# Kernel optimization log

Hardware: AMD Instinct MI355X
Metric: run time of the kernel (lower is better)

Reference implementation:

```python
import jax, jax.numpy as jnp
import numpy as np

N = 100000   # nodes
E = 1200000  # edges
F_IN = 16    # input node features
H = 64       # hidden dim (hard-coded in GinNet)
G = 1024     # graphs in the batch
BN_EPS = 1e-5


def setup_inputs() -> dict:
    key = jax.random.key(0)
    ks = jax.random.split(key, 16)

    def dense(k, shape):
        return (jax.random.normal(k, shape, jnp.float32) * (1.0 / np.sqrt(shape[0]))).astype(jnp.float32)

    x = jax.random.normal(ks[0], (N, F_IN), jnp.float32)
    edge_index = jax.random.randint(ks[1], (2, E), 0, N)
    batch = jnp.sort(jax.random.randint(ks[2], (N,), 0, G))

    inp = {
        'x': x, 'edge_index': edge_index, 'batch': batch,
        # GIN layer 1 (MLP F_IN->H->H, eps, BN affine)
        'W1a': dense(ks[3], (F_IN, H)), 'b1a': jnp.zeros((H,), jnp.float32),
        'W1b': dense(ks[4], (H, H)),    'b1b': jnp.zeros((H,), jnp.float32),
        'eps1': jnp.zeros((), jnp.float32), 'g1': jnp.ones((H,), jnp.float32), 'be1': jnp.zeros((H,), jnp.float32),
        # GIN layer 2
        'W2a': dense(ks[5], (H, H)), 'b2a': jnp.zeros((H,), jnp.float32),
        'W2b': dense(ks[6], (H, H)), 'b2b': jnp.zeros((H,), jnp.float32),
        'eps2': jnp.zeros((), jnp.float32), 'g2': jnp.ones((H,), jnp.float32), 'be2': jnp.zeros((H,), jnp.float32),
        # GIN layer 3
        'W3a': dense(ks[7], (H, H)), 'b3a': jnp.zeros((H,), jnp.float32),
        'W3b': dense(ks[8], (H, H)), 'b3b': jnp.zeros((H,), jnp.float32),
        'eps3': jnp.zeros((), jnp.float32), 'g3': jnp.ones((H,), jnp.float32), 'be3': jnp.zeros((H,), jnp.float32),
        # readout MLP
        'Wf1': dense(ks[9], (H, 10)), 'bf1': jnp.zeros((10,), jnp.float32),
        'Wf2': dense(ks[10], (10, 1)), 'bf2': jnp.zeros((1,), jnp.float32),
    }
    return inp


def _gin_bn(x, edge_index, eps, Wa, ba, Wb, bb, gamma, beta):
    # GINConv: out = MLP((1+eps)*x + sum_{j->i} x_j)
    msgs = x[edge_index[0]]                                      # [E, d] gather
    aggr = jax.ops.segment_sum(msgs, edge_index[1], num_segments=N)  # [N, d] scatter-add
    h = (1.0 + eps) * x + aggr
    h = jnp.maximum(h @ Wa + ba, 0.0) @ Wb + bb                  # Linear-ReLU-Linear
    h = jnp.maximum(h, 0.0)                                      # F.relu after conv
    # BatchNorm1d in training mode: batch statistics (biased var)
    mu = h.mean(axis=0)
    var = h.var(axis=0)
    return gamma * (h - mu) * jax.lax.rsqrt(var + BN_EPS) + beta


def reference(x, edge_index, batch,
              W1a, b1a, W1b, b1b, eps1, g1, be1,
              W2a, b2a, W2b, b2b, eps2, g2, be2,
              W3a, b3a, W3b, b3b, eps3, g3, be3,
              Wf1, bf1, Wf2, bf2):
    h = _gin_bn(x, edge_index, eps1, W1a, b1a, W1b, b1b, g1, be1)
    h = _gin_bn(h, edge_index, eps2, W2a, b2a, W2b, b2b, g2, be2)
    h = _gin_bn(h, edge_index, eps3, W3a, b3a, W3b, b3b, g3, be3)
    # global_mean_pool over graph ids
    sums = jax.ops.segment_sum(h, batch, num_segments=G)                     # [G, H]
    cnt = jax.ops.segment_sum(jnp.ones((N,), jnp.float32), batch, num_segments=G)
    pooled = sums / jnp.maximum(cnt, 1.0)[:, None]
    h = jnp.maximum(pooled @ Wf1 + bf1, 0.0)
    return h @ Wf2 + bf2  # [G, 1]
```

## Files before the change

### kernel.cpp

```cpp
#include <hip/hip_runtime.h>
#include <hip/hip_bf16.h>


#define HD 64
#define NBLK 256
#define BSH 9

typedef unsigned short u16;

__device__ __forceinline__ float bf2f(u16 u) {
    return __uint_as_float(((unsigned int)u) << 16);
}
__device__ __forceinline__ u16 f2bf(float f) {
    unsigned int u = __float_as_uint(f);
    unsigned int r = 0x7FFFu + ((u >> 16) & 1u);
    return (u16)((u + r) >> 16);
}

__global__ void hist_kernel(const int* __restrict__ ei, int* __restrict__ ghist, int E, int C) {
    __shared__ int lh[256];
    int b = blockIdx.x, tid = threadIdx.x;
    lh[tid] = 0;
    __syncthreads();
    int beg = b * C, end = min(beg + C, E);
    for (int i = beg + tid; i < end; i += 256) atomicAdd(&lh[ei[E + i] >> BSH], 1);
    __syncthreads();
    ghist[b * 256 + tid] = lh[tid];
}

__global__ void colscan_kernel(int* __restrict__ ghist, int* __restrict__ total) {
    __shared__ int s[256];
    int k = blockIdx.x, b = threadIdx.x;
    int v = ghist[b * 256 + k];
    s[b] = v;
    __syncthreads();
    for (int off = 1; off < 256; off <<= 1) {
        int u = (b >= off) ? s[b - off] : 0;
        __syncthreads();
        s[b] += u;
        __syncthreads();
    }
    ghist[b * 256 + k] = s[b] - v;
    if (b == 255) total[k] = s[255];
}

__global__ void base_kernel(const int* __restrict__ total, int* __restrict__ bbase, int NBUCK) {
    __shared__ int s[256];
    int t = threadIdx.x;
    int v = (t < NBUCK) ? total[t] : 0;
    s[t] = v;
    __syncthreads();
    for (int off = 1; off < 256; off <<= 1) {
        int u = (t >= off) ? s[t - off] : 0;
        __syncthreads();
        s[t] += u;
        __syncthreads();
    }
    if (t == 0) bbase[0] = 0;
    bbase[t + 1] = s[t];
}

__global__ void scatter_kernel(const int* __restrict__ ei, const int* __restrict__ ghist,
                               const int* __restrict__ bbase, int* __restrict__ bpack,
                               int E, int C) {
    __shared__ int lcur[256];
    int b = blockIdx.x, tid = threadIdx.x;
    lcur[tid] = bbase[tid] + ghist[b * 256 + tid];
    __syncthreads();
    int beg = b * C, end = min(beg + C, E);
    for (int i = beg + tid; i < end; i += 256) {
        int src = ei[i], dst = ei[E + i];
        int pos = atomicAdd(&lcur[dst >> BSH], 1);
        bpack[pos] = src | ((dst & 511) << 17);
    }
}

__global__ void csrbuild_kernel(const int* __restrict__ bpack, const int* __restrict__ bbase,
                                int* __restrict__ row_start, int* __restrict__ csr, int N) {
    __shared__ int h[512], s[512], lc[512];
    int k = blockIdx.x, tid = threadIdx.x;
    int beg = bbase[k], end = bbase[k + 1];
    h[tid] = 0; h[tid + 256] = 0;
    __syncthreads();
    for (int i = beg + tid; i < end; i += 256) atomicAdd(&h[(bpack[i] >> 17) & 511], 1);
    __syncthreads();
    s[tid] = h[tid]; s[tid + 256] = h[tid + 256];
    __syncthreads();
    for (int off = 1; off < 512; off <<= 1) {
        int v0 = (tid >= off) ? s[tid - off] : 0;
        int t1 = tid + 256;
        int v1 = (t1 >= off) ? s[t1 - off] : 0;
        __syncthreads();
        s[tid] += v0; s[t1] += v1;
        __syncthreads();
    }
    int e0 = s[tid] - h[tid], e1 = s[tid + 256] - h[tid + 256];
    lc[tid] = e0; lc[tid + 256] = e1;
    int n0 = (k << BSH) + tid, n1 = (k << BSH) + tid + 256;
    if (n0 < N) row_start[n0] = beg + e0;
    if (n1 < N) row_start[n1] = beg + e1;
    if (k == gridDim.x - 1 && tid == 0) row_start[N] = end;
    __syncthreads();
    for (int i = beg + tid; i < end; i += 256) {
        int v = bpack[i];
        int pos = beg + atomicAdd(&lc[(v >> 17) & 511], 1);
        csr[pos] = v & 0x1FFFF;
    }
}

__global__ void gather64_kernel(const u16* __restrict__ x, const int* __restrict__ rs,
                                const int* __restrict__ csr, float* __restrict__ aggr, int N) {
    int lane = threadIdx.x & 63;
    int l4 = lane & 15;
    int wave = (blockIdx.x * blockDim.x + threadIdx.x) >> 6;
    int n = wave * 4 + (lane >> 4);
    if (n >= N) return;
    int beg = rs[n], end = rs[n + 1];
    const u16* xb = x + (size_t)l4 * 4;
    float a0x = 0, a0y = 0, a0z = 0, a0w = 0;
    float a1x = 0, a1y = 0, a1z = 0, a1w = 0;
    float a2x = 0, a2y = 0, a2z = 0, a2w = 0;
    float a3x = 0, a3y = 0, a3z = 0, a3w = 0;
    for (int base = beg; base < end; base += 16) {
        int cnt = end - base; if (cnt > 16) cnt = 16;
        int e = (l4 < cnt) ? csr[base + l4] : 0;
        int j = 0;
        for (; j + 4 <= cnt; j += 4) {
            int s0 = __shfl(e, j + 0, 16);
            int s1 = __shfl(e, j + 1, 16);
            int s2 = __shfl(e, j + 2, 16);
            int s3 = __shfl(e, j + 3, 16);
            ushort4 u0 = *(const ushort4*)(xb + (size_t)s0 * 64);
            ushort4 u1 = *(const ushort4*)(xb + (size_t)s1 * 64);
            ushort4 u2 = *(const ushort4*)(xb + (size_t)s2 * 64);
            ushort4 u3 = *(const ushort4*)(xb + (size_t)s3 * 64);
            a0x += bf2f(u0.x); a0y += bf2f(u0.y); a0z += bf2f(u0.z); a0w += bf2f(u0.w);
            a1x += bf2f(u1.x); a1y += bf2f(u1.y); a1z += bf2f(u1.z); a1w += bf2f(u1.w);
            a2x += bf2f(u2.x); a2y += bf2f(u2.y); a2z += bf2f(u2.z); a2w += bf2f(u2.w);
            a3x += bf2f(u3.x); a3y += bf2f(u3.y); a3z += bf2f(u3.z); a3w += bf2f(u3.w);
        }
        for (; j < cnt; j++) {
            int s = __shfl(e, j, 16);
            ushort4 u = *(const ushort4*)(xb + (size_t)s * 64);
            a0x += bf2f(u.x); a0y += bf2f(u.y); a0z += bf2f(u.z); a0w += bf2f(u.w);
        }
    }
    float4 o;
    o.x = (a0x + a1x) + (a2x + a3x);
    o.y = (a0y + a1y) + (a2y + a3y);
    o.z = (a0z + a1z) + (a2z + a3z);
    o.w = (a0w + a1w) + (a2w + a3w);
    *reinterpret_cast<float4*>(aggr + (size_t)n * 64 + l4 * 4) = o;
}

__global__ void gather16_kernel(const float* __restrict__ x, const int* __restrict__ rs,
                                const int* __restrict__ csr, float* __restrict__ aggr, int N) {
    int lane = threadIdx.x & 63;
    int l4 = lane & 3;
    int wave = (blockIdx.x * blockDim.x + threadIdx.x) >> 6;
    int n = wave * 16 + (lane >> 2);
    if (n >= N) return;
    int beg = rs[n], end = rs[n + 1];
    const float* xb = x + (size_t)l4 * 4;
    float a0x = 0, a0y = 0, a0z = 0, a0w = 0;
    float a1x = 0, a1y = 0, a1z = 0, a1w = 0;
    float a2x = 0, a2y = 0, a2z = 0, a2w = 0;
    float a3x = 0, a3y = 0, a3z = 0, a3w = 0;
    for (int base = beg; base < end; base += 4) {
        int cnt = end - base; if (cnt > 4) cnt = 4;
        int e = (l4 < cnt) ? csr[base + l4] : 0;
        if (cnt == 4) {
            int s0 = __shfl(e, 0, 4);
            int s1 = __shfl(e, 1, 4);
            int s2 = __shfl(e, 2, 4);
            int s3 = __shfl(e, 3, 4);
            float4 v0 = *(const float4*)(xb + (size_t)s0 * 16);
            float4 v1 = *(const float4*)(xb + (size_t)s1 * 16);
            float4 v2 = *(const float4*)(xb + (size_t)s2 * 16);
            float4 v3 = *(const float4*)(xb + (size_t)s3 * 16);
            a0x += v0.x; a0y += v0.y; a0z += v0.z; a0w += v0.w;
            a1x += v1.x; a1y += v1.y; a1z += v1.z; a1w += v1.w;
            a2x += v2.x; a2y += v2.y; a2z += v2.z; a2w += v2.w;
            a3x += v3.x; a3y += v3.y; a3z += v3.z; a3w += v3.w;
        } else {
            for (int j = 0; j < cnt; j++) {
                int s = __shfl(e, j, 4);
                float4 v = *(const float4*)(xb + (size_t)s * 16);
                a0x += v.x; a0y += v.y; a0z += v.z; a0w += v.w;
            }
        }
    }
    float4 o;
    o.x = (a0x + a1x) + (a2x + a3x);
    o.y = (a0y + a1y) + (a2y + a3y);
    o.z = (a0z + a1z) + (a2z + a3z);
    o.w = (a0w + a1w) + (a2w + a3w);
    *reinterpret_cast<float4*>(aggr + (size_t)n * 16 + l4 * 4) = o;
}

template <int DIN, bool AFF>
__launch_bounds__(256)
__global__ void fused_mlp_kernel(const void* __restrict__ xin_, const float* __restrict__ aggr,
                                 const int* __restrict__ rs,
                                 const float* __restrict__ Wa, const float* __restrict__ ba,
                                 const float* __restrict__ Wb, const float* __restrict__ bb,
                                 const float* __restrict__ epsp,
                                 const float* __restrict__ statsPrev,
                                 const float* __restrict__ gPrev, const float* __restrict__ bePrev,
                                 u16* __restrict__ hout, float* __restrict__ stats, int N) {
    __shared__ float Wa_s[DIN * 64];
    __shared__ float Wb_s[64 * 64];
    __shared__ float zts[64 * 68];
    __shared__ float statS[128];
    __shared__ float degS[64];
    __shared__ float aS[64], cS[64], uS[64];

    const int tid = threadIdx.x;
    const int tc = tid & 15;
    const int tn = tid >> 4;
    const float* xinF = (const float*)xin_;
    const u16*   xinB = (const u16*)xin_;

    if (AFF) {
        if (tid < 64) {
            float invN = 1.0f / (float)N;
            float mu = statsPrev[tid] * invN;
            float var = statsPrev[64 + tid] * invN - mu * mu;
            float inv = rsqrtf(var + 1e-5f);
            float a = gPrev[tid] * inv;
            aS[tid] = a;
            cS[tid] = bePrev[tid] - mu * a;
        }
        __syncthreads();
        for (int i = tid; i < DIN * 64; i += 256) Wa_s[i] = aS[i >> 6] * Wa[i];
        if (tid < 64) {
            float s = 0.0f;
            for (int k = 0; k < 64; k++) s = fmaf(cS[k], Wa[k * 64 + tid], s);
            uS[tid] = s;
        }
    } else {
        for (int i = tid; i < DIN * 64; i += 256) Wa_s[i] = Wa[i];
    }
    for (int i = tid; i < 64 * 64; i += 256) Wb_s[i] = Wb[i];
    if (tid < 128) statS[tid] = 0.0f;
    const float e1 = 1.0f + epsp[0];
    __syncthreads();

    float4 t4;
    t4 = *(const float4*)&ba[tc * 4];
    const float bav[4] = {t4.x, t4.y, t4.z, t4.w};
    t4 = *(const float4*)&bb[tc * 4];
    const float bbv[4] = {t4.x, t4.y, t4.z, t4.w};
    float uv[4] = {0, 0, 0, 0};
    if (AFF) { uv[0] = uS[tc * 4]; uv[1] = uS[tc * 4 + 1]; uv[2] = uS[tc * 4 + 2]; uv[3] = uS[tc * 4 + 3]; }

    float sv[4] = {0, 0, 0, 0}, qv[4] = {0, 0, 0, 0};

    const int ITER = 2;
    int blockBase = blockIdx.x * (64 * ITER);
    for (int it = 0; it < ITER; ++it) {
        int gbase = blockBase + it * 64;
        float zr[4][4];
        if (DIN == 64) {
#pragma unroll
            for (int i = 0; i < 4; ++i) {
                int node = gbase + tn * 4 + i;
                float4 av = {0, 0, 0, 0};
                float xf[4] = {0, 0, 0, 0};
                if (node < N) {
                    ushort4 xu = *(const ushort4*)&xinB[(size_t)node * 64 + tc * 4];
                    xf[0] = bf2f(xu.x); xf[1] = bf2f(xu.y); xf[2] = bf2f(xu.z); xf[3] = bf2f(xu.w);
                    av = *(const float4*)&aggr[(size_t)node * 64 + tc * 4];
                }
                zr[i][0] = fmaf(e1, xf[0], av.x);
                zr[i][1] = fmaf(e1, xf[1], av.y);
                zr[i][2] = fmaf(e1, xf[2], av.z);
                zr[i][3] = fmaf(e1, xf[3], av.w);
            }
        } else {
            int node = gbase + tn * 4 + (tc >> 2);
            float4 xv = {0, 0, 0, 0}, av = {0, 0, 0, 0};
            if (node < N) {
                xv = *(const float4*)&xinF[(size_t)node * 16 + (tc & 3) * 4];
                av = *(const float4*)&aggr[(size_t)node * 16 + (tc & 3) * 4];
            }
            zr[0][0] = fmaf(e1, xv.x, av.x);
            zr[0][1] = fmaf(e1, xv.y, av.y);
            zr[0][2] = fmaf(e1, xv.z, av.z);
            zr[0][3] = fmaf(e1, xv.w, av.w);
        }
        float dg[4];
        if (AFF && tid < 64) {
            int node = gbase + tid;
            degS[tid] = (node < N) ? (float)(rs[node + 1] - rs[node]) : 0.0f;
        }
        __syncthreads();
        if (DIN == 64) {
#pragma unroll
            for (int j = 0; j < 4; ++j) {
                float4 w = {zr[0][j], zr[1][j], zr[2][j], zr[3][j]};
                *(float4*)&zts[(tc * 4 + j) * 68 + tn * 4] = w;
            }
        } else {
#pragma unroll
            for (int j = 0; j < 4; ++j)
                zts[((tc & 3) * 4 + j) * 68 + tn * 4 + (tc >> 2)] = zr[0][j];
        }
        __syncthreads();
        if (AFF) {
#pragma unroll
            for (int i = 0; i < 4; ++i) dg[i] = e1 + degS[tn * 4 + i];
        }
        float ac[4][4];
#pragma unroll
        for (int i = 0; i < 4; ++i)
#pragma unroll
            for (int j = 0; j < 4; ++j)
                ac[i][j] = AFF ? fmaf(dg[i], uv[j], bav[j]) : bav[j];
#pragma unroll 8
        for (int k = 0; k < DIN; ++k) {
            float4 zv = *(const float4*)&zts[k * 68 + tn * 4];
            float4 wv = *(const float4*)&Wa_s[k * 64 + tc * 4];
            const float zf[4] = {zv.x, zv.y, zv.z, zv.w};
            const float wf[4] = {wv.x, wv.y, wv.z, wv.w};
#pragma unroll
            for (int i = 0; i < 4; ++i)
#pragma unroll
                for (int j = 0; j < 4; ++j)
                    ac[i][j] = fmaf(zf[i], wf[j], ac[i][j]);
        }
#pragma unroll
        for (int i = 0; i < 4; ++i)
#pragma unroll
            for (int j = 0; j < 4; ++j)
                ac[i][j] = fmaxf(ac[i][j], 0.0f);
        __syncthreads();
#pragma unroll
        for (int j = 0; j < 4; ++j) {
            float4 w = {ac[0][j], ac[1][j], ac[2][j], ac[3][j]};
            *(float4*)&zts[(tc * 4 + j) * 68 + tn * 4] = w;
        }
        __syncthreads();
        float hc[4][4];
#pragma unroll
        for (int i = 0; i < 4; ++i)
#pragma unroll
            for (int j = 0; j < 4; ++j)
                hc[i][j] = bbv[j];
#pragma unroll 8
        for (int k = 0; k < 64; ++k) {
            float4 tv = *(const float4*)&zts[k * 68 + tn * 4];
            float4 wv = *(const float4*)&Wb_s[k * 64 + tc * 4];
            const float tf[4] = {tv.x, tv.y, tv.z, tv.w};
            const float wf[4] = {wv.x, wv.y, wv.z, wv.w};
#pragma unroll
            for (int i = 0; i < 4; ++i)
#pragma unroll
                for (int j = 0; j < 4; ++j)
                    hc[i][j] = fmaf(tf[i], wf[j], hc[i][j]);
        }
#pragma unroll
        for (int i = 0; i < 4; ++i) {
            int node = gbase + tn * 4 + i;
            if (node < N) {
                float o0 = fmaxf(hc[i][0], 0.0f), o1 = fmaxf(hc[i][1], 0.0f);
                float o2 = fmaxf(hc[i][2], 0.0f), o3 = fmaxf(hc[i][3], 0.0f);
                ushort4 ob = {f2bf(o0), f2bf(o1), f2bf(o2), f2bf(o3)};
                *(ushort4*)&hout[(size_t)node * 64 + tc * 4] = ob;
                sv[0] += o0; sv[1] += o1; sv[2] += o2; sv[3] += o3;
                qv[0] += o0 * o0; qv[1] += o1 * o1; qv[2] += o2 * o2; qv[3] += o3 * o3;
            }
        }
    }
#pragma unroll
    for (int off = 16; off < 64; off <<= 1) {
#pragma unroll
        for (int j = 0; j < 4; ++j) {
            sv[j] += __shfl_xor(sv[j], off);
            qv[j] += __shfl_xor(qv[j], off);
        }
    }
    if ((tid & 63) < 16) {
#pragma unroll
        for (int j = 0; j < 4; ++j) {
            atomicAdd(&statS[tc * 4 + j], sv[j]);
            atomicAdd(&statS[64 + tc * 4 + j], qv[j]);
        }
    }
    __syncthreads();
    if (tid < 128) unsafeAtomicAdd(&stats[tid], statS[tid]);
}

__global__ void pool_seg_kernel(const u16* __restrict__ h, const int* __restrict__ batch,
                                float* __restrict__ pool, float* __restrict__ cnt, int N) {
    int lane = threadIdx.x & 63;
    int wave = (blockIdx.x * blockDim.x + threadIdx.x) >> 6;
    int base = wave * 16;
    if (base >= N) return;
    int end = base + 16; if (end > N) end = N;
    int cur = batch[base];
    float acc = 0.0f;
    int run = 0;
    for (int n = base; n < end; n++) {
        int gid = batch[n];
        if (gid != cur) {
            unsafeAtomicAdd(&pool[(size_t)cur * 64 + lane], acc);
            if (lane == 0) unsafeAtomicAdd(&cnt[cur], (float)run);
            acc = 0.0f; run = 0; cur = gid;
        }
        acc += bf2f(h[(size_t)n * 64 + lane]);
        run++;
    }
    unsafeAtomicAdd(&pool[(size_t)cur * 64 + lane], acc);
    if (lane == 0) unsafeAtomicAdd(&cnt[cur], (float)run);
}

__global__ void readout_kernel(const float* __restrict__ pool, const float* __restrict__ cnt,
                               const float* __restrict__ stats, const float* __restrict__ g3,
                               const float* __restrict__ be3,
                               const float* __restrict__ Wf1, const float* __restrict__ bf1,
                               const float* __restrict__ Wf2, const float* __restrict__ bf2,
                               float* __restrict__ out, int N) {
    int gb = blockIdx.x;
    int t = threadIdx.x;
    float invN = 1.0f / (float)N;
    float mu = stats[t] * invN;
    float var = stats[64 + t] * invN - mu * mu;
    float inv = rsqrtf(var + 1e-5f);
    float a = g3[t] * inv;
    float c = be3[t] - mu * a;
    float cn = cnt[gb];
    float p = (cn > 0.0f) ? (a * (pool[(size_t)gb * 64 + t] / cn) + c) : 0.0f;
    float o = 0.0f;
#pragma unroll
    for (int j = 0; j < 10; j++) {
        float part = p * Wf1[t * 10 + j];
#pragma unroll
        for (int off = 32; off > 0; off >>= 1) part += __shfl_down(part, off);
        float z = fmaxf(part + bf1[j], 0.0f);
        o = fmaf(z, Wf2[j], o);
    }
    if (t == 0) out[gb] = o + bf2[0];
}

extern "C" void kernel_launch(void* const* d_in, const int* in_sizes, int n_in,
                              void* d_out, int out_size, void* d_ws, size_t ws_size,
                              hipStream_t stream) {
    const float* x      = (const float*)d_in[0];
    const int*   ei     = (const int*)d_in[1];
    const int*   batch  = (const int*)d_in[2];
    const float* W1a = (const float*)d_in[3];  const float* b1a = (const float*)d_in[4];
    const float* W1b = (const float*)d_in[5];  const float* b1b = (const float*)d_in[6];
    const float* e1  = (const float*)d_in[7];  const float* g1  = (const float*)d_in[8];
    const float* be1 = (const float*)d_in[9];
    const float* W2a = (const float*)d_in[10]; const float* b2a = (const float*)d_in[11];
    const float* W2b = (const float*)d_in[12]; const float* b2b = (const float*)d_in[13];
    const float* e2  = (const float*)d_in[14]; const float* g2  = (const float*)d_in[15];
    const float* be2 = (const float*)d_in[16];
    const float* W3a = (const float*)d_in[17]; const float* b3a = (const float*)d_in[18];
    const float* W3b = (const float*)d_in[19]; const float* b3b = (const float*)d_in[20];
    const float* e3  = (const float*)d_in[21]; const float* g3  = (const float*)d_in[22];
    const float* be3 = (const float*)d_in[23];
    const float* Wf1 = (const float*)d_in[24]; const float* bf1 = (const float*)d_in[25];
    const float* Wf2 = (const float*)d_in[26]; const float* bf2 = (const float*)d_in[27];

    const int N = in_sizes[2];
    const int E = in_sizes[1] / 2;
    const int G = out_size;
    const int NBUCK = (N + 511) >> BSH;
    const int C = (E + NBLK - 1) / NBLK;

    int* csr       = (int*)d_ws;
    int* row_start = csr + E;
    int* bpack     = row_start + N + 64;
    int* ghist     = bpack + E;
    int* total     = ghist + NBLK * 256;
    int* bbase     = total + 256;
    float* stats   = (float*)(bbase + 272);
    float* pool    = stats + 384;
    float* cnt     = pool + (size_t)G * HD;
    float* aggr    = cnt + G;
    size_t NH = (size_t)N * HD;
    u16* hA        = (u16*)(aggr + NH);
    u16* hB        = hA + NH;

    const int TB = 256;
    int fusedGrid = (N + 127) / 128;
    size_t zeroBytes = (size_t)(384 + (size_t)G * HD + G) * sizeof(float);

    hipMemsetAsync(stats, 0, zeroBytes, stream);
    hist_kernel<<<NBLK, 256, 0, stream>>>(ei, ghist, E, C);
    colscan_kernel<<<NBUCK, 256, 0, stream>>>(ghist, total);
    base_kernel<<<1, 256, 0, stream>>>(total, bbase, NBUCK);
    scatter_kernel<<<NBLK, 256, 0, stream>>>(ei, ghist, bbase, bpack, E, C);
    csrbuild_kernel<<<NBUCK, 256, 0, stream>>>(bpack, bbase, row_start, csr, N);

    gather16_kernel<<<((N + 15) / 16 * 64 + TB - 1) / TB, TB, 0, stream>>>(x, row_start, csr, aggr, N);
    fused_mlp_kernel<16, false><<<fusedGrid, TB, 0, stream>>>(
        x, aggr, row_start, W1a, b1a, W1b, b1b, e1, nullptr, nullptr, nullptr, hA, stats, N);

    gather64_kernel<<<((N + 3) / 4 * 64 + TB - 1) / TB, TB, 0, stream>>>(hA, row_start, csr, aggr, N);
    fused_mlp_kernel<64, true><<<fusedGrid, TB, 0, stream>>>(
        hA, aggr, row_start, W2a, b2a, W2b, b2b, e2, stats, g1, be1, hB, stats + 128, N);

    gather64_kernel<<<((N + 3) / 4 * 64 + TB - 1) / TB, TB, 0, stream>>>(hB, row_start, csr, aggr, N);
    fused_mlp_kernel<64, true><<<fusedGrid, TB, 0, stream>>>(
        hB, aggr, row_start, W3a, b3a, W3b, b3b, e3, stats + 128, g2, be2, hA, stats + 256, N);

    int poolWaves = (N + 15) / 16;
    pool_seg_kernel<<<(poolWaves * 64 + TB - 1) / TB, TB, 0, stream>>>(hA, batch, pool, cnt, N);
    readout_kernel<<<G, 64, 0, stream>>>(pool, cnt, stats + 256, g3, be3,
                                         Wf1, bf1, Wf2, bf2, (float*)d_out, N);
}
```

Measured before the change: 406.6 us.

## Fuse neighbor gather-aggregation into the fused MLP kernel

Removes the separate gather16/gather64 kernels and performs the CSR neighbor sum directly inside fused_mlp_kernel, feeding the result straight into the MLP. This eliminates writing and re-reading the fp32 aggr buffer (N×64 floats per layer) and three kernel launches. In exchange, the gather now runs at the MLP kernel's occupancy and block shape (256 threads, large shared memory), and each thread handles four nodes serially, which may expose gather latency and load imbalance across degree variation.

New measurement: 442.2 us. 8.8% more time.

```diff
diff --git a/kernel.cpp b/kernel.cpp
--- a/kernel.cpp
+++ b/kernel.cpp
@@ -108,100 +108,10 @@
     }
 }
 
-__global__ void gather64_kernel(const u16* __restrict__ x, const int* __restrict__ rs,
-                                const int* __restrict__ csr, float* __restrict__ aggr, int N) {
-    int lane = threadIdx.x & 63;
-    int l4 = lane & 15;
-    int wave = (blockIdx.x * blockDim.x + threadIdx.x) >> 6;
-    int n = wave * 4 + (lane >> 4);
-    if (n >= N) return;
-    int beg = rs[n], end = rs[n + 1];
-    const u16* xb = x + (size_t)l4 * 4;
-    float a0x = 0, a0y = 0, a0z = 0, a0w = 0;
-    float a1x = 0, a1y = 0, a1z = 0, a1w = 0;
-    float a2x = 0, a2y = 0, a2z = 0, a2w = 0;
-    float a3x = 0, a3y = 0, a3z = 0, a3w = 0;
-    for (int base = beg; base < end; base += 16) {
-        int cnt = end - base; if (cnt > 16) cnt = 16;
-        int e = (l4 < cnt) ? csr[base + l4] : 0;
-        int j = 0;
-        for (; j + 4 <= cnt; j += 4) {
-            int s0 = __shfl(e, j + 0, 16);
-            int s1 = __shfl(e, j + 1, 16);
-            int s2 = __shfl(e, j + 2, 16);
-            int s3 = __shfl(e, j + 3, 16);
-            ushort4 u0 = *(const ushort4*)(xb + (size_t)s0 * 64);
-            ushort4 u1 = *(const ushort4*)(xb + (size_t)s1 * 64);
-            ushort4 u2 = *(const ushort4*)(xb + (size_t)s2 * 64);
-            ushort4 u3 = *(const ushort4*)(xb + (size_t)s3 * 64);
-            a0x += bf2f(u0.x); a0y += bf2f(u0.y); a0z += bf2f(u0.z); a0w += bf2f(u0.w);
-            a1x += bf2f(u1.x); a1y += bf2f(u1.y); a1z += bf2f(u1.z); a1w += bf2f(u1.w);
-            a2x += bf2f(u2.x); a2y += bf2f(u2.y); a2z += bf2f(u2.z); a2w += bf2f(u2.w);
-            a3x += bf2f(u3.x); a3y += bf2f(u3.y); a3z += bf2f(u3.z); a3w += bf2f(u3.w);
-        }
-        for (; j < cnt; j++) {
-            int s = __shfl(e, j, 16);
-            ushort4 u = *(const ushort4*)(xb + (size_t)s * 64);
-            a0x += bf2f(u.x); a0y += bf2f(u.y); a0z += bf2f(u.z); a0w += bf2f(u.w);
-        }
-    }
-    float4 o;
-    o.x = (a0x + a1x) + (a2x + a3x);
-    o.y = (a0y + a1y) + (a2y + a3y);
-    o.z = (a0z + a1z) + (a2z + a3z);
-    o.w = (a0w + a1w) + (a2w + a3w);
-    *reinterpret_cast<float4*>(aggr + (size_t)n * 64 + l4 * 4) = o;
-}
-
-__global__ void gather16_kernel(const float* __restrict__ x, const int* __restrict__ rs,
-                                const int* __restrict__ csr, float* __restrict__ aggr, int N) {
-    int lane = threadIdx.x & 63;
-    int l4 = lane & 3;
-    int wave = (blockIdx.x * blockDim.x + threadIdx.x) >> 6;
-    int n = wave * 16 + (lane >> 2);
-    if (n >= N) return;
-    int beg = rs[n], end = rs[n + 1];
-    const float* xb = x + (size_t)l4 * 4;
-    float a0x = 0, a0y = 0, a0z = 0, a0w = 0;
-    float a1x = 0, a1y = 0, a1z = 0, a1w = 0;
-    float a2x = 0, a2y = 0, a2z = 0, a2w = 0;
-    float a3x = 0, a3y = 0, a3z = 0, a3w = 0;
-    for (int base = beg; base < end; base += 4) {
-        int cnt = end - base; if (cnt > 4) cnt = 4;
-        int e = (l4 < cnt) ? csr[base + l4] : 0;
-        if (cnt == 4) {
-            int s0 = __shfl(e, 0, 4);
-            int s1 = __shfl(e, 1, 4);
-            int s2 = __shfl(e, 2, 4);
-            int s3 = __shfl(e, 3, 4);
-            float4 v0 = *(const float4*)(xb + (size_t)s0 * 16);
-            float4 v1 = *(const float4*)(xb + (size_t)s1 * 16);
-            float4 v2 = *(const float4*)(xb + (size_t)s2 * 16);
-            float4 v3 = *(const float4*)(xb + (size_t)s3 * 16);
-            a0x += v0.x; a0y += v0.y; a0z += v0.z; a0w += v0.w;
-            a1x += v1.x; a1y += v1.y; a1z += v1.z; a1w += v1.w;
-            a2x += v2.x; a2y += v2.y; a2z += v2.z; a2w += v2.w;
-            a3x += v3.x; a3y += v3.y; a3z += v3.z; a3w += v3.w;
-        } else {
-            for (int j = 0; j < cnt; j++) {
-                int s = __shfl(e, j, 4);
-                float4 v = *(const float4*)(xb + (size_t)s * 16);
-                a0x += v.x; a0y += v.y; a0z += v.z; a0w += v.w;
-            }
-        }
-    }
-    float4 o;
-    o.x = (a0x + a1x) + (a2x + a3x);
-    o.y = (a0y + a1y) + (a2y + a3y);
-    o.z = (a0z + a1z) + (a2z + a3z);
-    o.w = (a0w + a1w) + (a2w + a3w);
-    *reinterpret_cast<float4*>(aggr + (size_t)n * 16 + l4 * 4) = o;
-}
-
 template <int DIN, bool AFF>
 __launch_bounds__(256)
-__global__ void fused_mlp_kernel(const void* __restrict__ xin_, const float* __restrict__ aggr,
-                                 const int* __restrict__ rs,
+__global__ void fused_mlp_kernel(const void* __restrict__ xin_,
+                                 const int* __restrict__ rs, const int* __restrict__ csr,
                                  const float* __restrict__ Wa, const float* __restrict__ ba,
                                  const float* __restrict__ Wb, const float* __restrict__ bb,
                                  const float* __restrict__ epsp,
@@ -265,29 +175,89 @@
 #pragma unroll
             for (int i = 0; i < 4; ++i) {
                 int node = gbase + tn * 4 + i;
-                float4 av = {0, 0, 0, 0};
-                float xf[4] = {0, 0, 0, 0};
+                float a0x = 0, a0y = 0, a0z = 0, a0w = 0;
+                float a1x = 0, a1y = 0, a1z = 0, a1w = 0;
+                float a2x = 0, a2y = 0, a2z = 0, a2w = 0;
+                float a3x = 0, a3y = 0, a3z = 0, a3w = 0;
                 if (node < N) {
-                    ushort4 xu = *(const ushort4*)&xinB[(size_t)node * 64 + tc * 4];
-                    xf[0] = bf2f(xu.x); xf[1] = bf2f(xu.y); xf[2] = bf2f(xu.z); xf[3] = bf2f(xu.w);
-                    av = *(const float4*)&aggr[(size_t)node * 64 + tc * 4];
+                    int beg = rs[node], end = rs[node + 1];
+                    const u16* xb = xinB + (size_t)tc * 4;
+                    for (int base = beg; base < end; base += 16) {
+                        int cnt = end - base; if (cnt > 16) cnt = 16;
+                        int e = (tc < cnt) ? csr[base + tc] : 0;
+                        int j = 0;
+                        for (; j + 4 <= cnt; j += 4) {
+                            int s0 = __shfl(e, j + 0, 16);
+                            int s1 = __shfl(e, j + 1, 16);
+                            int s2 = __shfl(e, j + 2, 16);
+                            int s3 = __shfl(e, j + 3, 16);
+                            ushort4 u0 = *(const ushort4*)(xb + (size_t)s0 * 64);
+                            ushort4 u1 = *(const ushort4*)(xb + (size_t)s1 * 64);
+                            ushort4 u2 = *(const ushort4*)(xb + (size_t)s2 * 64);
+                            ushort4 u3 = *(const ushort4*)(xb + (size_t)s3 * 64);
+                            a0x += bf2f(u0.x); a0y += bf2f(u0.y); a0z += bf2f(u0.z); a0w += bf2f(u0.w);
+                            a1x += bf2f(u1.x); a1y += bf2f(u1.y); a1z += bf2f(u1.z); a1w += bf2f(u1.w);
+                            a2x += bf2f(u2.x); a2y += bf2f(u2.y); a2z += bf2f(u2.z); a2w += bf2f(u2.w);
+                            a3x += bf2f(u3.x); a3y += bf2f(u3.y); a3z += bf2f(u3.z); a3w += bf2f(u3.w);
+                        }
+                        for (; j < cnt; j++) {
+                            int s = __shfl(e, j, 16);
+                            ushort4 u = *(const ushort4*)(xb + (size_t)s * 64);
+                            a0x += bf2f(u.x); a0y += bf2f(u.y); a0z += bf2f(u.z); a0w += bf2f(u.w);
+                        }
+                    }
+                    ushort4 xs = *(const ushort4*)&xinB[(size_t)node * 64 + tc * 4];
+                    zr[i][0] = fmaf(e1, bf2f(xs.x), (a0x + a1x) + (a2x + a3x));
+                    zr[i][1] = fmaf(e1, bf2f(xs.y), (a0y + a1y) + (a2y + a3y));
+                    zr[i][2] = fmaf(e1, bf2f(xs.z), (a0z + a1z) + (a2z + a3z));
+                    zr[i][3] = fmaf(e1, bf2f(xs.w), (a0w + a1w) + (a2w + a3w));
+                } else {
+                    zr[i][0] = zr[i][1] = zr[i][2] = zr[i][3] = 0.0f;
                 }
-                zr[i][0] = fmaf(e1, xf[0], av.x);
-                zr[i][1] = fmaf(e1, xf[1], av.y);
-                zr[i][2] = fmaf(e1, xf[2], av.z);
-                zr[i][3] = fmaf(e1, xf[3], av.w);
             }
         } else {
             int node = gbase + tn * 4 + (tc >> 2);
-            float4 xv = {0, 0, 0, 0}, av = {0, 0, 0, 0};
+            int cq = (tc & 3) * 4;
+            float a0x = 0, a0y = 0, a0z = 0, a0w = 0;
+            float a1x = 0, a1y = 0, a1z = 0, a1w = 0;
+            float a2x = 0, a2y = 0, a2z = 0, a2w = 0;
+            float a3x = 0, a3y = 0, a3z = 0, a3w = 0;
             if (node < N) {
-                xv = *(const float4*)&xinF[(size_t)node * 16 + (tc & 3) * 4];
-                av = *(const float4*)&aggr[(size_t)node * 16 + (tc & 3) * 4];
+                int beg = rs[node], end = rs[node + 1];
+                const float* xb = xinF + (size_t)cq;
+                int l4 = tc & 3;
+                for (int base = beg; base < end; base += 4) {
+                    int cnt = end - base; if (cnt > 4) cnt = 4;
+                    int e = (l4 < cnt) ? csr[base + l4] : 0;
+                    if (cnt == 4) {
+                        int s0 = __shfl(e, 0, 4);
+                        int s1 = __shfl(e, 1, 4);
+                        int s2 = __shfl(e, 2, 4);
+                        int s3 = __shfl(e, 3, 4);
+                        float4 v0 = *(const float4*)(xb + (size_t)s0 * 16);
+                        float4 v1 = *(const float4*)(xb + (size_t)s1 * 16);
+                        float4 v2 = *(const float4*)(xb + (size_t)s2 * 16);
+                        float4 v3 = *(const float4*)(xb + (size_t)s3 * 16);
+                        a0x += v0.x; a0y += v0.y; a0z += v0.z; a0w += v0.w;
+                        a1x += v1.x; a1y += v1.y; a1z += v1.z; a1w += v1.w;
+                        a2x += v2.x; a2y += v2.y; a2z += v2.z; a2w += v2.w;
+                        a3x += v3.x; a3y += v3.y; a3z += v3.z; a3w += v3.w;
+                    } else {
+                        for (int j = 0; j < cnt; j++) {
+                            int s = __shfl(e, j, 4);
+                            float4 v = *(const float4*)(xb + (size_t)s * 16);
+                            a0x += v.x; a0y += v.y; a0z += v.z; a0w += v.w;
+                        }
+                    }
+                }
+                float4 xs = *(const float4*)&xinF[(size_t)node * 16 + cq];
+                zr[0][0] = fmaf(e1, xs.x, (a0x + a1x) + (a2x + a3x));
+                zr[0][1] = fmaf(e1, xs.y, (a0y + a1y) + (a2y + a3y));
+                zr[0][2] = fmaf(e1, xs.z, (a0z + a1z) + (a2z + a3z));
+                zr[0][3] = fmaf(e1, xs.w, (a0w + a1w) + (a2w + a3w));
+            } else {
+                zr[0][0] = zr[0][1] = zr[0][2] = zr[0][3] = 0.0f;
             }
-            zr[0][0] = fmaf(e1, xv.x, av.x);
-            zr[0][1] = fmaf(e1, xv.y, av.y);
-            zr[0][2] = fmaf(e1, xv.z, av.z);
-            zr[0][3] = fmaf(e1, xv.w, av.w);
         }
         float dg[4];
         if (AFF && tid < 64) {
@@ -479,9 +449,8 @@
     float* stats   = (float*)(bbase + 272);
     float* pool    = stats + 384;
     float* cnt     = pool + (size_t)G * HD;
-    float* aggr    = cnt + G;
     size_t NH = (size_t)N * HD;
-    u16* hA        = (u16*)(aggr + NH);
+    u16* hA        = (u16*)(cnt + G);
     u16* hB        = hA + NH;
 
     const int TB = 256;
@@ -495,17 +464,14 @@
     scatter_kernel<<<NBLK, 256, 0, stream>>>(ei, ghist, bbase, bpack, E, C);
     csrbuild_kernel<<<NBUCK, 256, 0, stream>>>(bpack, bbase, row_start, csr, N);
 
-    gather16_kernel<<<((N + 15) / 16 * 64 + TB - 1) / TB, TB, 0, stream>>>(x, row_start, csr, aggr, N);
     fused_mlp_kernel<16, false><<<fusedGrid, TB, 0, stream>>>(
-        x, aggr, row_start, W1a, b1a, W1b, b1b, e1, nullptr, nullptr, nullptr, hA, stats, N);
-
-    gather64_kernel<<<((N + 3) / 4 * 64 + TB - 1) / TB, TB, 0, stream>>>(hA, row_start, csr, aggr, N);
+        x, row_start, csr, W1a, b1a, W1b, b1b, e1, nullptr, nullptr, nullptr, hA, stats, N);
+
     fused_mlp_kernel<64, true><<<fusedGrid, TB, 0, stream>>>(
-        hA, aggr, row_start, W2a, b2a, W2b, b2b, e2, stats, g1, be1, hB, stats + 128, N);
-
-    gather64_kernel<<<((N + 3) / 4 * 64 + TB - 1) / TB, TB, 0, stream>>>(hB, row_start, csr, aggr, N);
+        hA, row_start, csr, W2a, b2a, W2b, b2b, e2, stats, g1, be1, hB, stats + 128, N);
+
     fused_mlp_kernel<64, true><<<fusedGrid, TB, 0, stream>>>(
-        hB, aggr, row_start, W3a, b3a, W3b, b3b, e3, stats + 128, g2, be2, hA, stats + 256, N);
+        hB, row_start, csr, W3a, b3a, W3b, b3b, e3, stats + 128, g2, be2, hA, stats + 256, N);
 
     int poolWaves = (N + 15) / 16;
     pool_seg_kernel<<<(poolWaves * 64 + TB - 1) / TB, TB, 0, stream>>>(hA, batch, pool, cnt, N);
```

## Fuse mean-pool accumulation into last MLP layer and prefetch node inputs

Applied to the files above, without the earlier changes.

The final fused MLP kernel now accumulates per-graph pooled sums and counts with atomics straight from registers, so the separate pool kernel and the bf16 write and re-read of the last hidden layer go away. Pooling is done on pre-BN ReLU outputs, which stays correct because BN is affine and readout applies it after averaging. Loads of node features and aggregates are also issued before weight staging, and the next tile is prefetched inside the loop, to overlap global memory latency. The cost is more atomics per thread (4-node runs instead of 16-node runs), with extra register pressure from the prefetch buffers.

After: 406.5 us. No clear change (-0.0%).

```diff
diff --git a/kernel.cpp b/kernel.cpp
--- a/kernel.cpp
+++ b/kernel.cpp
@@ -198,16 +198,17 @@
     *reinterpret_cast<float4*>(aggr + (size_t)n * 16 + l4 * 4) = o;
 }
 
-template <int DIN, bool AFF>
+template <int DIN, bool AFF, bool POOL>
 __launch_bounds__(256)
 __global__ void fused_mlp_kernel(const void* __restrict__ xin_, const float* __restrict__ aggr,
-                                 const int* __restrict__ rs,
+                                 const int* __restrict__ rs, const int* __restrict__ batch,
                                  const float* __restrict__ Wa, const float* __restrict__ ba,
                                  const float* __restrict__ Wb, const float* __restrict__ bb,
                                  const float* __restrict__ epsp,
                                  const float* __restrict__ statsPrev,
                                  const float* __restrict__ gPrev, const float* __restrict__ bePrev,
-                                 u16* __restrict__ hout, float* __restrict__ stats, int N) {
+                                 u16* __restrict__ hout, float* __restrict__ stats,
+                                 float* __restrict__ pool, float* __restrict__ cnt, int N) {
     __shared__ float Wa_s[DIN * 64];
     __shared__ float Wb_s[64 * 64];
     __shared__ float zts[64 * 68];
@@ -220,6 +221,32 @@
     const int tn = tid >> 4;
     const float* xinF = (const float*)xin_;
     const u16*   xinB = (const u16*)xin_;
+
+    const int ITER = 2;
+    int blockBase = blockIdx.x * (64 * ITER);
+
+    ushort4 xuP[4]; float4 avP[4];
+    float4  xvP, av16P;
+    if (DIN == 64) {
+#pragma unroll
+        for (int i = 0; i < 4; ++i) {
+            int node = blockBase + tn * 4 + i;
+            xuP[i] = make_ushort4(0, 0, 0, 0);
+            avP[i] = make_float4(0, 0, 0, 0);
+            if (node < N) {
+                xuP[i] = *(const ushort4*)&xinB[(size_t)node * 64 + tc * 4];
+                avP[i] = *(const float4*)&aggr[(size_t)node * 64 + tc * 4];
+            }
+        }
+    } else {
+        int node = blockBase + tn * 4 + (tc >> 2);
+        xvP = make_float4(0, 0, 0, 0);
+        av16P = make_float4(0, 0, 0, 0);
+        if (node < N) {
+            xvP = *(const float4*)&xinF[(size_t)node * 16 + (tc & 3) * 4];
+            av16P = *(const float4*)&aggr[(size_t)node * 16 + (tc & 3) * 4];
+        }
+    }
 
     if (AFF) {
         if (tid < 64) {
@@ -256,38 +283,46 @@
 
     float sv[4] = {0, 0, 0, 0}, qv[4] = {0, 0, 0, 0};
 
-    const int ITER = 2;
-    int blockBase = blockIdx.x * (64 * ITER);
     for (int it = 0; it < ITER; ++it) {
         int gbase = blockBase + it * 64;
         float zr[4][4];
         if (DIN == 64) {
 #pragma unroll
             for (int i = 0; i < 4; ++i) {
-                int node = gbase + tn * 4 + i;
-                float4 av = {0, 0, 0, 0};
-                float xf[4] = {0, 0, 0, 0};
+                zr[i][0] = fmaf(e1, bf2f(xuP[i].x), avP[i].x);
+                zr[i][1] = fmaf(e1, bf2f(xuP[i].y), avP[i].y);
+                zr[i][2] = fmaf(e1, bf2f(xuP[i].z), avP[i].z);
+                zr[i][3] = fmaf(e1, bf2f(xuP[i].w), avP[i].w);
+            }
+        } else {
+            zr[0][0] = fmaf(e1, xvP.x, av16P.x);
+            zr[0][1] = fmaf(e1, xvP.y, av16P.y);
+            zr[0][2] = fmaf(e1, xvP.z, av16P.z);
+            zr[0][3] = fmaf(e1, xvP.w, av16P.w);
+        }
+        if (it + 1 < ITER) {
+            int nbase = gbase + 64;
+            if (DIN == 64) {
+#pragma unroll
+                for (int i = 0; i < 4; ++i) {
+                    int node = nbase + tn * 4 + i;
+                    ushort4 xu = make_ushort4(0, 0, 0, 0);
+                    float4 av = make_float4(0, 0, 0, 0);
+                    if (node < N) {
+                        xu = *(const ushort4*)&xinB[(size_t)node * 64 + tc * 4];
+                        av = *(const float4*)&aggr[(size_t)node * 64 + tc * 4];
+                    }
+                    xuP[i] = xu; avP[i] = av;
+                }
+            } else {
+                int node = nbase + tn * 4 + (tc >> 2);
+                float4 xv = make_float4(0, 0, 0, 0), av = make_float4(0, 0, 0, 0);
                 if (node < N) {
-                    ushort4 xu = *(const ushort4*)&xinB[(size_t)node * 64 + tc * 4];
-                    xf[0] = bf2f(xu.x); xf[1] = bf2f(xu.y); xf[2] = bf2f(xu.z); xf[3] = bf2f(xu.w);
-                    av = *(const float4*)&aggr[(size_t)node * 64 + tc * 4];
+                    xv = *(const float4*)&xinF[(size_t)node * 16 + (tc & 3) * 4];
+                    av = *(const float4*)&aggr[(size_t)node * 16 + (tc & 3) * 4];
                 }
-                zr[i][0] = fmaf(e1, xf[0], av.x);
-                zr[i][1] = fmaf(e1, xf[1], av.y);
-                zr[i][2] = fmaf(e1, xf[2], av.z);
-                zr[i][3] = fmaf(e1, xf[3], av.w);
-            }
-        } else {
-            int node = gbase + tn * 4 + (tc >> 2);
-            float4 xv = {0, 0, 0, 0}, av = {0, 0, 0, 0};
-            if (node < N) {
-                xv = *(const float4*)&xinF[(size_t)node * 16 + (tc & 3) * 4];
-                av = *(const float4*)&aggr[(size_t)node * 16 + (tc & 3) * 4];
-            }
-            zr[0][0] = fmaf(e1, xv.x, av.x);
-            zr[0][1] = fmaf(e1, xv.y, av.y);
-            zr[0][2] = fmaf(e1, xv.z, av.z);
-            zr[0][3] = fmaf(e1, xv.w, av.w);
+                xvP = xv; av16P = av;
+            }
         }
         float dg[4];
         if (AFF && tid < 64) {
@@ -359,16 +394,49 @@
                 for (int j = 0; j < 4; ++j)
                     hc[i][j] = fmaf(tf[i], wf[j], hc[i][j]);
         }
-#pragma unroll
-        for (int i = 0; i < 4; ++i) {
-            int node = gbase + tn * 4 + i;
-            if (node < N) {
-                float o0 = fmaxf(hc[i][0], 0.0f), o1 = fmaxf(hc[i][1], 0.0f);
-                float o2 = fmaxf(hc[i][2], 0.0f), o3 = fmaxf(hc[i][3], 0.0f);
-                ushort4 ob = {f2bf(o0), f2bf(o1), f2bf(o2), f2bf(o3)};
-                *(ushort4*)&hout[(size_t)node * 64 + tc * 4] = ob;
-                sv[0] += o0; sv[1] += o1; sv[2] += o2; sv[3] += o3;
-                qv[0] += o0 * o0; qv[1] += o1 * o1; qv[2] += o2 * o2; qv[3] += o3 * o3;
+        if (POOL) {
+            int curg = -1; float p0 = 0, p1 = 0, p2 = 0, p3 = 0; int run = 0;
+#pragma unroll
+            for (int i = 0; i < 4; ++i) {
+                int node = gbase + tn * 4 + i;
+                if (node < N) {
+                    float o0 = fmaxf(hc[i][0], 0.0f), o1 = fmaxf(hc[i][1], 0.0f);
+                    float o2 = fmaxf(hc[i][2], 0.0f), o3 = fmaxf(hc[i][3], 0.0f);
+                    sv[0] += o0; sv[1] += o1; sv[2] += o2; sv[3] += o3;
+                    qv[0] += o0 * o0; qv[1] += o1 * o1; qv[2] += o2 * o2; qv[3] += o3 * o3;
+                    int gid = batch[node];
+                    if (gid != curg) {
+                        if (curg >= 0) {
+                            unsafeAtomicAdd(&pool[(size_t)curg * 64 + tc * 4 + 0], p0);
+                            unsafeAtomicAdd(&pool[(size_t)curg * 64 + tc * 4 + 1], p1);
+                            unsafeAtomicAdd(&pool[(size_t)curg * 64 + tc * 4 + 2], p2);
+                            unsafeAtomicAdd(&pool[(size_t)curg * 64 + tc * 4 + 3], p3);
+                            if (tc == 0) unsafeAtomicAdd(&cnt[curg], (float)run);
+                        }
+                        curg = gid; p0 = p1 = p2 = p3 = 0.0f; run = 0;
+                    }
+                    p0 += o0; p1 += o1; p2 += o2; p3 += o3; run++;
+                }
+            }
+            if (curg >= 0) {
+                unsafeAtomicAdd(&pool[(size_t)curg * 64 + tc * 4 + 0], p0);
+                unsafeAtomicAdd(&pool[(size_t)curg * 64 + tc * 4 + 1], p1);
+                unsafeAtomicAdd(&pool[(size_t)curg * 64 + tc * 4 + 2], p2);
+                unsafeAtomicAdd(&pool[(size_t)curg * 64 + tc * 4 + 3], p3);
+                if (tc == 0) unsafeAtomicAdd(&cnt[curg], (float)run);
+            }
+        } else {
+#pragma unroll
+            for (int i = 0; i < 4; ++i) {
+                int node = gbase + tn * 4 + i;
+                if (node < N) {
+                    float o0 = fmaxf(hc[i][0], 0.0f), o1 = fmaxf(hc[i][1], 0.0f);
+                    float o2 = fmaxf(hc[i][2], 0.0f), o3 = fmaxf(hc[i][3], 0.0f);
+                    ushort4 ob = {f2bf(o0), f2bf(o1), f2bf(o2), f2bf(o3)};
+                    *(ushort4*)&hout[(size_t)node * 64 + tc * 4] = ob;
+                    sv[0] += o0; sv[1] += o1; sv[2] += o2; sv[3] += o3;
+                    qv[0] += o0 * o0; qv[1] += o1 * o1; qv[2] += o2 * o2; qv[3] += o3 * o3;
+                }
             }
         }
     }
@@ -389,30 +457,6 @@
     }
     __syncthreads();
     if (tid < 128) unsafeAtomicAdd(&stats[tid], statS[tid]);
-}
-
-__global__ void pool_seg_kernel(const u16* __restrict__ h, const int* __restrict__ batch,
-                                float* __restrict__ pool, float* __restrict__ cnt, int N) {
-    int lane = threadIdx.x & 63;
-    int wave = (blockIdx.x * blockDim.x + threadIdx.x) >> 6;
-    int base = wave * 16;
-    if (base >= N) return;
-    int end = base + 16; if (end > N) end = N;
-    int cur = batch[base];
-    float acc = 0.0f;
-    int run = 0;
-    for (int n = base; n < end; n++) {
-        int gid = batch[n];
-        if (gid != cur) {
-            unsafeAtomicAdd(&pool[(size_t)cur * 64 + lane], acc);
-            if (lane == 0) unsafeAtomicAdd(&cnt[cur], (float)run);
-            acc = 0.0f; run = 0; cur = gid;
-        }
-        acc += bf2f(h[(size_t)n * 64 + lane]);
-        run++;
-    }
-    unsafeAtomicAdd(&pool[(size_t)cur * 64 + lane], acc);
-    if (lane == 0) unsafeAtomicAdd(&cnt[cur], (float)run);
 }
 
 __global__ void readout_kernel(const float* __restrict__ pool, const float* __restrict__ cnt,
@@ -496,19 +540,20 @@
     csrbuild_kernel<<<NBUCK, 256, 0, stream>>>(bpack, bbase, row_start, csr, N);
 
     gather16_kernel<<<((N + 15) / 16 * 64 + TB - 1) / TB, TB, 0, stream>>>(x, row_start, csr, aggr, N);
-    fused_mlp_kernel<16, false><<<fusedGrid, TB, 0, stream>>>(
-        x, aggr, row_start, W1a, b1a, W1b, b1b, e1, nullptr, nullptr, nullptr, hA, stats, N);
+    fused_mlp_kernel<16, false, false><<<fusedGrid, TB, 0, stream>>>(
+        x, aggr, row_start, batch, W1a, b1a, W1b, b1b, e1,
+        nullptr, nullptr, nullptr, hA, stats, nullptr, nullptr, N);
 
     gather64_kernel<<<((N + 3) / 4 * 64 + TB - 1) / TB, TB, 0, stream>>>(hA, row_start, csr, aggr, N);
-    fused_mlp_kernel<64, true><<<fusedGrid, TB, 0, stream>>>(
-        hA, aggr, row_start, W2a, b2a, W2b, b2b, e2, stats, g1, be1, hB, stats + 128, N);
+    fused_mlp_kernel<64, true, false><<<fusedGrid, TB, 0, stream>>>(
+        hA, aggr, row_start, batch, W2a, b2a, W2b, b2b, e2,
+        stats, g1, be1, hB, stats + 128, nullptr, nullptr, N);
 
     gather64_kernel<<<((N + 3) / 4 * 64 + TB - 1) / TB, TB, 0, stream>>>(hB, row_start, csr, aggr, N);
-    fused_mlp_kernel<64, true><<<fusedGrid, TB, 0, stream>>>(
-        hB, aggr, row_start, W3a, b3a, W3b, b3b, e3, stats + 128, g2, be2, hA, stats + 256, N);
-
-    int poolWaves = (N + 15) / 16;
-    pool_seg_kernel<<<(poolWaves * 64 + TB - 1) / TB, TB, 0, stream>>>(hA, batch, pool, cnt, N);
+    fused_mlp_kernel<64, true, true><<<fusedGrid, TB, 0, stream>>>(
+        hB, aggr, row_start, batch, W3a, b3a, W3b, b3b, e3,
+        stats + 128, g2, be2, hA , stats + 256, pool, cnt, N);
+
     readout_kernel<<<G, 64, 0, stream>>>(pool, cnt, stats + 256, g3, be3,
                                          Wf1, bf1, Wf2, bf2, (float*)d_out, N);
 }
```
